# Performance work log

Hardware: AMD Instinct MI355X
Metric: run time of the kernel (lower is better)

## Reference

```python
import jax, jax.numpy as jnp
import numpy as np
from jax import lax

LR, SB, LB = 256, 16, 8  # lr_size, spatial_bin, luma_bins
DN = ('NCHW', 'OIHW', 'NCHW')


def conv2d(x, w, b=None, stride=1, pad=1):
    out = lax.conv_general_dilated(x, w, (stride, stride), [(pad, pad), (pad, pad)], dimension_numbers=DN)
    return out if b is None else out + b[None, :, None, None]


def gaussian_blur17(x):
    # kornia GaussianBlur2d(kernel=(17,17), sigma=(2,2)), reflect padding, separable
    t = jnp.arange(17, dtype=x.dtype) - 8.0
    g = jnp.exp(-(t * t) / 8.0)  # 2*sigma^2 = 8
    g = g / g.sum()
    C = x.shape[1]
    xp = jnp.pad(x, ((0, 0), (0, 0), (8, 8), (8, 8)), mode='reflect')
    kh = jnp.broadcast_to(g.reshape(1, 1, 17, 1), (C, 1, 17, 1))
    kw = jnp.broadcast_to(g.reshape(1, 1, 1, 17), (C, 1, 1, 17))
    x1 = lax.conv_general_dilated(xp, kh, (1, 1), 'VALID', dimension_numbers=DN, feature_group_count=C)
    return lax.conv_general_dilated(x1, kw, (1, 1), 'VALID', dimension_numbers=DN, feature_group_count=C)


def nearest_resize(x, size):
    # torch F.interpolate mode='nearest': src = floor(dst * in/out)
    H, W = x.shape[-2], x.shape[-1]
    iy = jnp.floor(jnp.arange(size) * (H / size)).astype(jnp.int32)
    ix = jnp.floor(jnp.arange(size) * (W / size)).astype(jnp.int32)
    return x[:, :, iy][:, :, :, ix]


def grid_sample_3d_border(inp, grid):
    # inp [B,C,D,Hi,Wi]; grid [B,Do,Ho,Wo,3] with (x,y,z); bilinear, padding_mode='border', align_corners=False
    B, C, D, Hi, Wi = inp.shape
    x = jnp.clip(((grid[..., 0] + 1.0) * Wi - 1.0) * 0.5, 0.0, Wi - 1.0)
    y = jnp.clip(((grid[..., 1] + 1.0) * Hi - 1.0) * 0.5, 0.0, Hi - 1.0)
    z = jnp.clip(((grid[..., 2] + 1.0) * D - 1.0) * 0.5, 0.0, D - 1.0)
    x0 = jnp.floor(x); y0 = jnp.floor(y); z0 = jnp.floor(z)
    fx = (x - x0)[:, None]; fy = (y - y0)[:, None]; fz = (z - z0)[:, None]  # [B,1,Do,Ho,Wo]
    x0i = x0.astype(jnp.int32); y0i = y0.astype(jnp.int32); z0i = z0.astype(jnp.int32)
    x1i = jnp.minimum(x0i + 1, Wi - 1); y1i = jnp.minimum(y0i + 1, Hi - 1); z1i = jnp.minimum(z0i + 1, D - 1)
    flat = inp.reshape(B, C, D * Hi * Wi)
    M = grid.shape[1] * grid.shape[2] * grid.shape[3]

    def gat(zi, yi, xi):
        idx = ((zi * Hi + yi) * Wi + xi).reshape(B, 1, M)
        v = jnp.take_along_axis(flat, jnp.broadcast_to(idx, (B, C, M)), axis=2)
        return v.reshape(B, C, grid.shape[1], grid.shape[2], grid.shape[3])

    return (gat(z0i, y0i, x0i) * (1 - fz) * (1 - fy) * (1 - fx)
            + gat(z0i, y0i, x1i) * (1 - fz) * (1 - fy) * fx
            + gat(z0i, y1i, x0i) * (1 - fz) * fy * (1 - fx)
            + gat(z0i, y1i, x1i) * (1 - fz) * fy * fx
            + gat(z1i, y0i, x0i) * fz * (1 - fy) * (1 - fx)
            + gat(z1i, y0i, x1i) * fz * (1 - fy) * fx
            + gat(z1i, y1i, x0i) * fz * fy * (1 - fx)
            + gat(z1i, y1i, x1i) * fz * fy * fx)


def _forward(lqs, evs, gw1, gb1, gw2, gb2, sw0, sb0, sw1, sb1, sw2, sb2, sw3, sb3,
             cw0, cb0, cw1, cb1, fw1, fb1, fw2, fb2, fw3, fb3, lw1, lb1, lw2, fuw, fub):
    B, _, H, W = lqs.shape
    # --- HighresStreamNet guide ---
    g = gaussian_blur17(lqs)
    g = jax.nn.relu(conv2d(g, gw1, gb1, 1, 0))
    guide = jax.nn.sigmoid(conv2d(g, gw2, gb2, 1, 0)) * 2.0 - 0.5  # [B,1,H,W]
    # --- slicing grid (x,y in (-0.5,1.5) per source, z = guide) ---
    gx = (jnp.arange(W, dtype=lqs.dtype) + 0.5) / W * 2.0 - 0.5
    gy = (jnp.arange(H, dtype=lqs.dtype) + 0.5) / H * 2.0 - 0.5
    gyy, gxx = jnp.meshgrid(gy, gx, indexing='ij')
    base = jnp.broadcast_to(jnp.stack([gxx, gyy], -1)[None, None], (B, 1, H, W, 2))
    grid = jnp.concatenate([base, guide[..., None]], axis=-1)  # [B,1,H,W,3]
    # --- LowresStreamNet ---
    lr = nearest_resize(lqs, LR)
    ev = evs if (evs.shape[-1] == LR and evs.shape[-2] == LR) else nearest_resize(evs, LR)
    x = jnp.concatenate([lr, ev], axis=1)  # [B,18,256,256]
    for w_, b_ in ((sw0, sb0), (sw1, sb1), (sw2, sb2), (sw3, sb3)):
        x = jax.nn.relu(conv2d(x, w_, b_, 2, 1))  # -> [B,64,16,16]
    xl = conv2d(jax.nn.relu(conv2d(x, lw1, lb1, 1, 1)), lw2, None, 1, 1)  # local, last conv no bias
    xg = jax.nn.relu(conv2d(x, cw0, cb0, 2, 1))
    xg = jax.nn.relu(conv2d(xg, cw1, cb1, 2, 1)).reshape(B, -1)  # [B,1024]
    xg = jax.nn.relu(xg @ fw1.T + fb1)
    xg = jax.nn.relu(xg @ fw2.T + fb2)
    xg = xg @ fw3.T + fb3  # [B,64]
    fused = jax.nn.relu(xg[:, :, None, None] + xl)
    bg = conv2d(fused, fuw, fub, 1, 0).reshape(B, 1, LB, SB, SB)  # bilateral grid [B,1,8,16,16]
    hr = grid_sample_3d_border(bg, grid)  # [B,1,1,H,W]
    return hr.reshape(B, -1, H, W)


def setup_inputs():
    key = jax.random.key(0)
    ks = iter(jax.random.split(key, 40))

    def W_(shape):
        fan_in = int(np.prod(shape[1:]))
        return jax.random.normal(next(ks), shape, jnp.float32) * np.float32(np.sqrt(2.0 / fan_in))

    def Z(n):
        return jnp.zeros((n,), jnp.float32)

    B, H, Wd = 8, 1024, 1024
    return {
        'lqs': jax.random.uniform(next(ks), (B, 3, H, Wd), jnp.float32),
        'evs': jax.random.normal(next(ks), (B, 15, 256, 256), jnp.float32) * 0.1,
        'gw1': W_((16, 3, 1, 1)), 'gb1': Z(16), 'gw2': W_((1, 16, 1, 1)), 'gb2': Z(1),
        'sw0': W_((8, 18, 3, 3)), 'sb0': Z(8), 'sw1': W_((16, 8, 3, 3)), 'sb1': Z(16),
        'sw2': W_((32, 16, 3, 3)), 'sb2': Z(32), 'sw3': W_((64, 32, 3, 3)), 'sb3': Z(64),
        'cw0': W_((64, 64, 3, 3)), 'cb0': Z(64), 'cw1': W_((64, 64, 3, 3)), 'cb1': Z(64),
        'fw1': W_((256, 1024)), 'fb1': Z(256), 'fw2': W_((128, 256)), 'fb2': Z(128),
        'fw3': W_((64, 128)), 'fb3': Z(64),
        'lw1': W_((64, 64, 3, 3)), 'lb1': Z(64), 'lw2': W_((64, 64, 3, 3)),
        'fuw': W_((8, 64, 1, 1)), 'fub': Z(8),
    }


def reference(lqs, evs, gw1, gb1, gw2, gb2, sw0, sb0, sw1, sb1, sw2, sb2, sw3, sb3,
              cw0, cb0, cw1, cb1, fw1, fb1, fw2, fb2, fw3, fb3, lw1, lb1, lw2, fuw, fub):
    return _forward(lqs, evs, gw1, gb1, gw2, gb2, sw0, sb0, sw1, sb1, sw2, sb2, sw3, sb3,
                    cw0, cb0, cw1, cb1, fw1, fb1, fw2, fb2, fw3, fb3, lw1, lb1, lw2, fuw, fub)
```

## Files before the change

### kernel.cpp

```cpp
#include <hip/hip_runtime.h>
#include <hip/hip_bf16.h>
#include <math.h>

#define BATCH 8
#define HH 1024
#define WW 1024

__device__ __forceinline__ int reflect1024(int i) {
    i = i < 0 ? -i : i;
    return i > 1023 ? 2046 - i : i;
}

__global__ __launch_bounds__(256) void conv0_k(const float* __restrict__ lqs,
                                               const float* __restrict__ evs,
                                               const float* __restrict__ w,
                                               const float* __restrict__ bias,
                                               float* __restrict__ out) {
    int idx = blockIdx.x * 256 + threadIdx.x;
    int q = idx & 4095;
    int b = idx >> 12;
    int qx = q & 31, oy = q >> 5;
    int iy0 = oy * 2 - 1;

    float acc[4][8];
#pragma unroll
    for (int j = 0; j < 4; ++j)
#pragma unroll
        for (int o = 0; o < 8; ++o) acc[j][o] = bias[o];

#pragma unroll
    for (int ic = 0; ic < 3; ++ic) {
        const float* ipc = lqs + (size_t)(b * 3 + ic) * HH * WW;
#pragma unroll
        for (int ky = 0; ky < 3; ++ky) {
            int iy = iy0 + ky;
            if (iy < 0) continue;
            const float* row = ipc + (size_t)iy * 4 * WW;
            float xr[9];
#pragma unroll
            for (int i = 0; i < 9; ++i) {
                int ix = 8 * qx - 1 + i;
                xr[i] = (ix >= 0) ? row[ix * 4] : 0.0f;
            }
#pragma unroll
            for (int o = 0; o < 8; ++o) {
                const float* wp = w + (o * 18 + ic) * 9 + ky * 3;
#pragma unroll
                for (int j = 0; j < 4; ++j)
#pragma unroll
                    for (int kx = 0; kx < 3; ++kx)
                        acc[j][o] = fmaf(wp[kx], xr[2 * j + kx], acc[j][o]);
            }
        }
    }
    for (int ic = 0; ic < 15; ++ic) {
        const float* ipc = evs + (size_t)(b * 15 + ic) * 65536;
#pragma unroll
        for (int ky = 0; ky < 3; ++ky) {
            int iy = iy0 + ky;
            if (iy < 0) continue;
            const float* row = ipc + iy * 256;
            const float4* r4 = (const float4*)row;
            float4 A = r4[2 * qx];
            float4 Bv = r4[2 * qx + 1];
            float m = (qx > 0) ? row[8 * qx - 1] : 0.0f;
            float xr[9] = {m, A.x, A.y, A.z, A.w, Bv.x, Bv.y, Bv.z, Bv.w};
#pragma unroll
            for (int o = 0; o < 8; ++o) {
                const float* wp = w + (o * 18 + ic + 3) * 9 + ky * 3;
#pragma unroll
                for (int j = 0; j < 4; ++j)
#pragma unroll
                    for (int kx = 0; kx < 3; ++kx)
                        acc[j][o] = fmaf(wp[kx], xr[2 * j + kx], acc[j][o]);
            }
        }
    }
#pragma unroll
    for (int o = 0; o < 8; ++o) {
        float4 v = make_float4(fmaxf(acc[0][o], 0.0f), fmaxf(acc[1][o], 0.0f),
                               fmaxf(acc[2][o], 0.0f), fmaxf(acc[3][o], 0.0f));
        *(float4*)(out + ((size_t)(b * 8 + o) << 14) + oy * 128 + qx * 4) = v;
    }
}

template <int IC, int OC, int OCT, int IH, int IW, int STRIDE, bool RELU, bool HASB>
__global__ __launch_bounds__(256) void convN_k(const float* __restrict__ in,
                                               const float* __restrict__ w,
                                               const float* __restrict__ bias,
                                               float* __restrict__ out) {
    constexpr int OH = (IH + 2 - 3) / STRIDE + 1;
    constexpr int OW = (IW + 2 - 3) / STRIDE + 1;
    constexpr int POS = OH * OW;
    constexpr int G = OC / OCT;
    int idx = blockIdx.x * 256 + threadIdx.x;
    if (idx >= BATCH * G * POS) return;
    int px = idx % POS;
    int g = (idx / POS) % G;
    int b = idx / (POS * G);
    int ox = px % OW, oy = px / OW;
    int iy0 = oy * STRIDE - 1, ix0 = ox * STRIDE - 1;

    float acc[OCT];
#pragma unroll
    for (int o = 0; o < OCT; ++o) acc[o] = HASB ? bias[g * OCT + o] : 0.0f;

    const float* ip = in + (size_t)b * IC * IH * IW;
    for (int ic = 0; ic < IC; ++ic) {
        const float* ipc = ip + ic * IH * IW;
        float x[9];
#pragma unroll
        for (int ky = 0; ky < 3; ++ky) {
            int iy = iy0 + ky;
#pragma unroll
            for (int kx = 0; kx < 3; ++kx) {
                int ix = ix0 + kx;
                bool ok = (iy >= 0) && (iy < IH) && (ix >= 0) && (ix < IW);
                x[ky * 3 + kx] = ok ? ipc[iy * IW + ix] : 0.0f;
            }
        }
#pragma unroll
        for (int o = 0; o < OCT; ++o) {
            const float* wp = w + ((g * OCT + o) * IC + ic) * 9;
#pragma unroll
            for (int k = 0; k < 9; ++k) acc[o] = fmaf(wp[k], x[k], acc[o]);
        }
    }
#pragma unroll
    for (int o = 0; o < OCT; ++o) {
        float v = acc[o];
        if (RELU) v = fmaxf(v, 0.0f);
        out[(size_t)(b * OC + g * OCT + o) * POS + px] = v;
    }
}

template <int IC, int OC, int OCT, int IH, int IW, int STRIDE, int SPLIT>
__global__ __launch_bounds__(256) void convS_k(const float* __restrict__ in,
                                               const float* __restrict__ w,
                                               float* __restrict__ part) {
    constexpr int OH = (IH + 2 - 3) / STRIDE + 1;
    constexpr int OW = (IW + 2 - 3) / STRIDE + 1;
    constexpr int POS = OH * OW;
    constexpr int G = OC / OCT;
    constexpr int TOT = BATCH * G * POS;
    constexpr int ICS = IC / SPLIT;
    constexpr int N = BATCH * OC * POS;
    int idx = blockIdx.x * 256 + threadIdx.x;
    if (idx >= TOT * SPLIT) return;
    int s = idx / TOT, r = idx % TOT;
    int px = r % POS;
    int g = (r / POS) % G;
    int b = r / (POS * G);
    int ox = px % OW, oy = px / OW;
    int iy0 = oy * STRIDE - 1, ix0 = ox * STRIDE - 1;

    float acc[OCT];
#pragma unroll
    for (int o = 0; o < OCT; ++o) acc[o] = 0.0f;

    const float* ip = in + (size_t)b * IC * IH * IW;
    for (int ic = s * ICS; ic < (s + 1) * ICS; ++ic) {
        const float* ipc = ip + ic * IH * IW;
        float x[9];
#pragma unroll
        for (int ky = 0; ky < 3; ++ky) {
            int iy = iy0 + ky;
#pragma unroll
            for (int kx = 0; kx < 3; ++kx) {
                int ix = ix0 + kx;
                bool ok = (iy >= 0) && (iy < IH) && (ix >= 0) && (ix < IW);
                x[ky * 3 + kx] = ok ? ipc[iy * IW + ix] : 0.0f;
            }
        }
#pragma unroll
        for (int o = 0; o < OCT; ++o) {
            const float* wp = w + ((g * OCT + o) * IC + ic) * 9;
#pragma unroll
            for (int k = 0; k < 9; ++k) acc[o] = fmaf(wp[k], x[k], acc[o]);
        }
    }
#pragma unroll
    for (int o = 0; o < OCT; ++o)
        part[(size_t)s * N + (size_t)(b * OC + g * OCT + o) * POS + px] = acc[o];
}

template <int OC, int POS, int SPLIT, bool RELU, bool HASB>
__global__ __launch_bounds__(256) void reduce_k(const float* __restrict__ part,
                                                const float* __restrict__ bias,
                                                float* __restrict__ out) {
    constexpr int N = BATCH * OC * POS;
    int idx = blockIdx.x * 256 + threadIdx.x;
    if (idx >= N) return;
    int oc = (idx / POS) % OC;
    float a = HASB ? bias[oc] : 0.0f;
#pragma unroll
    for (int s = 0; s < SPLIT; ++s) a += part[(size_t)s * N + idx];
    out[idx] = RELU ? fmaxf(a, 0.0f) : a;
}

__global__ __launch_bounds__(256) void fc1_k(const float* __restrict__ part_cw1,
                                             const float* __restrict__ cb1,
                                             const float* __restrict__ fw1,
                                             const float* __restrict__ fb1,
                                             float* __restrict__ h1) {
    __shared__ float xin[1024];
    int t = threadIdx.x;
    int b = blockIdx.x >> 6;
    int rgrp = blockIdx.x & 63;
    int wave = t >> 6, lane = t & 63;

    for (int i = t; i < 1024; i += 256) {
        float v = cb1[i >> 4];
#pragma unroll
        for (int s = 0; s < 16; ++s) v += part_cw1[s * 8192 + b * 1024 + i];
        xin[i] = fmaxf(v, 0.0f);
    }
    __syncthreads();

    int r = (rgrp << 2) | wave;
    const float4* w4 = (const float4*)(fw1 + r * 1024);
    const float4* x4 = (const float4*)xin;
    float acc = 0.0f;
#pragma unroll
    for (int jj = 0; jj < 4; ++jj) {
        float4 wv = w4[lane + 64 * jj];
        float4 xv = x4[lane + 64 * jj];
        acc = fmaf(wv.x, xv.x, acc);
        acc = fmaf(wv.y, xv.y, acc);
        acc = fmaf(wv.z, xv.z, acc);
        acc = fmaf(wv.w, xv.w, acc);
    }
#pragma unroll
    for (int m = 32; m; m >>= 1) acc += __shfl_xor(acc, m, 64);
    if (lane == 0) h1[b * 256 + r] = fmaxf(acc + fb1[r], 0.0f);
}

__global__ __launch_bounds__(256) void fc23fuse_k(const float* __restrict__ h1,
                                                  const float* __restrict__ fw2,
                                                  const float* __restrict__ fb2,
                                                  const float* __restrict__ fw3,
                                                  const float* __restrict__ fb3,
                                                  const float* __restrict__ part_lw2,
                                                  const float* __restrict__ fuw,
                                                  const float* __restrict__ fub,
                                                  float* __restrict__ bg) {
    __shared__ float h2[128];
    __shared__ float xg[64];
    int b = blockIdx.x, t = threadIdx.x;
    int wave = t >> 6, lane = t & 63;

    float4 xv1 = ((const float4*)(h1 + b * 256))[lane];
#pragma unroll 4
    for (int i = 0; i < 32; ++i) {
        int r = wave * 32 + i;
        float4 wv = ((const float4*)(fw2 + r * 256))[lane];
        float acc = fmaf(wv.x, xv1.x, fmaf(wv.y, xv1.y, fmaf(wv.z, xv1.z, wv.w * xv1.w)));
#pragma unroll
        for (int m = 32; m; m >>= 1) acc += __shfl_xor(acc, m, 64);
        if (lane == 0) h2[r] = fmaxf(acc + fb2[r], 0.0f);
    }
    __syncthreads();

    float2 xv2 = ((const float2*)h2)[lane];
#pragma unroll 4
    for (int i = 0; i < 16; ++i) {
        int r = wave * 16 + i;
        float2 wv = ((const float2*)(fw3 + r * 128))[lane];
        float acc = fmaf(wv.x, xv2.x, wv.y * xv2.y);
#pragma unroll
        for (int m = 32; m; m >>= 1) acc += __shfl_xor(acc, m, 64);
        if (lane == 0) xg[r] = acc + fb3[r];
    }
    __syncthreads();

    int px = t;
    float acc[8];
#pragma unroll
    for (int d = 0; d < 8; ++d) acc[d] = fub[d];
    for (int c = 0; c < 64; ++c) {
        int base = (b * 64 + c) * 256 + px;
        float xlv = 0.0f;
#pragma unroll
        for (int s = 0; s < 8; ++s) xlv += part_lw2[s * 131072 + base];
        float f = fmaxf(xg[c] + xlv, 0.0f);
#pragma unroll
        for (int d = 0; d < 8; ++d) acc[d] = fmaf(fuw[d * 64 + c], f, acc[d]);
    }
#pragma unroll
    for (int d = 0; d < 8; ++d) bg[(b * 8 + d) * 256 + px] = acc[d];
}

__global__ __launch_bounds__(256) void guide_slice_k(const float* __restrict__ lqs,
                                                     const float* __restrict__ bgp,
                                                     const float* __restrict__ gw1,
                                                     const float* __restrict__ gb1,
                                                     const float* __restrict__ gw2,
                                                     const float* __restrict__ gb2,
                                                     float* __restrict__ out) {
    constexpr int TW = 64, TH = 32;
    __shared__ float sBH[3][TH][81];
    __shared__ float sBG[2048];
    __shared__ float sW1[48], sB1[16], sW2[16], sB2v[1];

    int t = threadIdx.x;
    int bx = blockIdx.x & 15;
    int by = (blockIdx.x >> 4) & 31;
    int b = blockIdx.x >> 9;
    int x0 = bx * TW, y0 = by * TH;

    float gv[17];
    {
        float gs = 0.0f;
#pragma unroll
        for (int i = 0; i < 17; ++i) {
            float d = (float)i - 8.0f;
            gv[i] = expf(-(d * d) * 0.125f);
            gs += gv[i];
        }
        float inv = 1.0f / gs;
#pragma unroll
        for (int i = 0; i < 17; ++i) gv[i] *= inv;
    }

    for (int i = t; i < 2048; i += 256) sBG[i] = bgp[b * 2048 + i];
    if (t < 48) sW1[t] = gw1[t];
    if (t < 16) { sB1[t] = gb1[t]; sW2[t] = gw2[t]; }
    if (t == 0) sB2v[0] = gb2[0];

    if (t < 240) {
        int c = t / 80, xo = t % 80;
        int gx = reflect1024(x0 + xo - 8);
        const float* colp = lqs + (size_t)(b * 3 + c) * HH * WW + gx;
        float win[17];
#pragma unroll
        for (int i = 0; i < 16; ++i)
            win[i] = colp[(size_t)reflect1024(y0 - 8 + i) * WW];
#pragma unroll
        for (int j = 0; j < TH; ++j) {
            win[(16 + j) % 17] = colp[(size_t)reflect1024(y0 + 8 + j) * WW];
            float acc = 0.0f;
#pragma unroll
            for (int i = 0; i < 17; ++i) acc = fmaf(gv[i], win[(j + i) % 17], acc);
            sBH[c][j][xo] = acc;
        }
    }
    __syncthreads();

    int yy = t >> 3, xs = (t & 7) * 8;
    int Y = y0 + yy;
    float fy = fminf(fmaxf((Y + 0.5f) * (1.0f / 64.0f) + 3.5f, 0.0f), 15.0f);
    float yf = floorf(fy);
    int yi = (int)yf;
    float ay = fy - yf;
    int yi1 = min(yi + 1, 15);

    float bcv[3][8];
#pragma unroll
    for (int c = 0; c < 3; ++c) {
        float win[17];
#pragma unroll
        for (int i = 0; i < 16; ++i) win[i] = sBH[c][yy][xs + i];
#pragma unroll
        for (int j = 0; j < 8; ++j) {
            win[(16 + j) % 17] = sBH[c][yy][xs + 16 + j];
            float acc = 0.0f;
#pragma unroll
            for (int i = 0; i < 17; ++i) acc = fmaf(gv[i], win[(j + i) % 17], acc);
            bcv[c][j] = acc;
        }
    }

    float val[8];
#pragma unroll
    for (int j = 0; j < 8; ++j) {
        float b0 = bcv[0][j], b1 = bcv[1][j], b2 = bcv[2][j];
        float s = sB2v[0];
#pragma unroll
        for (int c = 0; c < 16; ++c) {
            float g1 = fmaf(sW1[c * 3 + 0], b0,
                       fmaf(sW1[c * 3 + 1], b1,
                       fmaf(sW1[c * 3 + 2], b2, sB1[c])));
            s = fmaf(sW2[c], fmaxf(g1, 0.0f), s);
        }
        float sig = 1.0f / (1.0f + expf(-s));
        float guide = sig * 2.0f - 0.5f;

        int X = x0 + xs + j;
        float fx = fminf(fmaxf((X + 0.5f) * (1.0f / 64.0f) + 3.5f, 0.0f), 15.0f);
        float fz = fminf(fmaxf(fmaf(guide, 4.0f, 3.5f), 0.0f), 7.0f);
        float xf = floorf(fx), zf = floorf(fz);
        int xi = (int)xf, zi = (int)zf;
        float ax = fx - xf, az = fz - zf;
        int xi1 = min(xi + 1, 15), zi1 = min(zi + 1, 7);

        const float* g0 = sBG + zi * 256;
        const float* g1p = sBG + zi1 * 256;
        int i00 = yi * 16 + xi, i01 = yi * 16 + xi1;
        int i10 = yi1 * 16 + xi, i11 = yi1 * 16 + xi1;
        float c00 = g0[i00] + az * (g1p[i00] - g0[i00]);
        float c01 = g0[i01] + az * (g1p[i01] - g0[i01]);
        float c10 = g0[i10] + az * (g1p[i10] - g0[i10]);
        float c11 = g0[i11] + az * (g1p[i11] - g0[i11]);
        float c0 = c00 + ay * (c10 - c00);
        float c1 = c01 + ay * (c11 - c01);
        val[j] = c0 + ax * (c1 - c0);
    }
    float4* op = (float4*)(out + (size_t)b * HH * WW + (size_t)Y * WW + x0 + xs);
    op[0] = make_float4(val[0], val[1], val[2], val[3]);
    op[1] = make_float4(val[4], val[5], val[6], val[7]);
}

extern "C" void kernel_launch(void* const* d_in, const int* in_sizes, int n_in,
                              void* d_out, int out_size, void* d_ws, size_t ws_size,
                              hipStream_t stream) {
    const float* lqs = (const float*)d_in[0];
    const float* evs = (const float*)d_in[1];
    const float* gw1 = (const float*)d_in[2];
    const float* gb1 = (const float*)d_in[3];
    const float* gw2 = (const float*)d_in[4];
    const float* gb2 = (const float*)d_in[5];
    const float* sw0 = (const float*)d_in[6];
    const float* sb0 = (const float*)d_in[7];
    const float* sw1 = (const float*)d_in[8];
    const float* sb1 = (const float*)d_in[9];
    const float* sw2 = (const float*)d_in[10];
    const float* sb2 = (const float*)d_in[11];
    const float* sw3 = (const float*)d_in[12];
    const float* sb3 = (const float*)d_in[13];
    const float* cw0 = (const float*)d_in[14];
    const float* cb0 = (const float*)d_in[15];
    const float* cw1 = (const float*)d_in[16];
    const float* cb1 = (const float*)d_in[17];
    const float* fw1 = (const float*)d_in[18];
    const float* fb1 = (const float*)d_in[19];
    const float* fw2 = (const float*)d_in[20];
    const float* fb2 = (const float*)d_in[21];
    const float* fw3 = (const float*)d_in[22];
    const float* fb3 = (const float*)d_in[23];
    const float* lw1 = (const float*)d_in[24];
    const float* lb1 = (const float*)d_in[25];
    const float* lw2 = (const float*)d_in[26];
    const float* fuw = (const float*)d_in[27];
    const float* fub = (const float*)d_in[28];
    float* out = (float*)d_out;

    float* ws = (float*)d_ws;
    float* o0 = ws;
    float* o1 = o0 + 1048576;
    float* o2 = o1 + 524288;
    float* o3 = o2 + 262144;
    float* xl1 = o3 + 131072;
    float* xg0 = xl1 + 131072;
    float* h1 = xg0 + 32768;
    float* bg = h1 + 2048;
    float* partA = bg + 16384;
    float* part_lw2 = partA + 1048576;
    float* part_cw1 = part_lw2 + 1048576;

    conv0_k<<<128, 256, 0, stream>>>(lqs, evs, sw0, sb0, o0);
    convN_k<8, 16, 8, 128, 128, 2, true, true><<<256, 256, 0, stream>>>(o0, sw1, sb1, o1);
    convS_k<16, 32, 8, 64, 64, 2, 4><<<512, 256, 0, stream>>>(o1, sw2, partA);
    reduce_k<32, 1024, 4, true, true><<<1024, 256, 0, stream>>>(partA, sb2, o2);
    convS_k<32, 64, 8, 32, 32, 2, 8><<<512, 256, 0, stream>>>(o2, sw3, partA);
    reduce_k<64, 256, 8, true, true><<<512, 256, 0, stream>>>(partA, sb3, o3);
    convS_k<64, 64, 8, 16, 16, 1, 8><<<512, 256, 0, stream>>>(o3, lw1, partA);
    reduce_k<64, 256, 8, true, true><<<512, 256, 0, stream>>>(partA, lb1, xl1);
    convS_k<64, 64, 8, 16, 16, 1, 8><<<512, 256, 0, stream>>>(xl1, lw2, part_lw2);
    convS_k<64, 64, 8, 16, 16, 2, 16><<<256, 256, 0, stream>>>(o3, cw0, partA);
    reduce_k<64, 64, 16, true, true><<<128, 256, 0, stream>>>(partA, cb0, xg0);
    convS_k<64, 64, 4, 8, 8, 2, 16><<<128, 256, 0, stream>>>(xg0, cw1, part_cw1);
    fc1_k<<<512, 256, 0, stream>>>(part_cw1, cb1, fw1, fb1, h1);
    fc23fuse_k<<<8, 256, 0, stream>>>(h1, fw2, fb2, fw3, fb3, part_lw2, fuw, fub, bg);
    guide_slice_k<<<BATCH * 32 * 16, 256, 0, stream>>>(lqs, bg, gw1, gb1, gw2, gb2, out);
}
```

Before: 431.2 us.

## Fuse pipeline into persistent megakernel with grid barriers and overlapped guide blur

Replaces the fifteen separate launches with one persistent kernel of 768 blocks that walks the stages, separated by a software grid barrier built on atomics. The expensive 17x17 blur and guide MLP move out of the final slice kernel and are spread across the early, under-filled conv stages, so they overlap with the small convolutions. The guide z-coordinate is stored as a 16-bit fixed-point value and read back by a lighter slice pass. This removes launch gaps and idle tails. In exchange it adds barrier cost, depends on all 768 blocks being co-resident to avoid deadlock, loses some precision from the z quantization, and adds the extra global write and read of the quantized guide.

```diff
diff --git a/kernel.cpp b/kernel.cpp
--- a/kernel.cpp
+++ b/kernel.cpp
@@ -5,18 +5,37 @@
 #define BATCH 8
 #define HH 1024
 #define WW 1024
+#define NB 768
 
 __device__ __forceinline__ int reflect1024(int i) {
     i = i < 0 ? -i : i;
     return i > 1023 ? 2046 - i : i;
 }
 
-__global__ __launch_bounds__(256) void conv0_k(const float* __restrict__ lqs,
-                                               const float* __restrict__ evs,
-                                               const float* __restrict__ w,
-                                               const float* __restrict__ bias,
-                                               float* __restrict__ out) {
-    int idx = blockIdx.x * 256 + threadIdx.x;
+__device__ __forceinline__ void gridbar(unsigned int* cnt, unsigned int* gen) {
+    __syncthreads();
+    if (threadIdx.x == 0) {
+        __threadfence();
+        unsigned int g = atomicAdd(gen, 0u);
+        unsigned int a = atomicAdd(cnt, 1u);
+        if (a == NB - 1) {
+            atomicExch(cnt, 0u);
+            __threadfence();
+            atomicAdd(gen, 1u);
+        } else {
+            while (atomicAdd(gen, 0u) == g) __builtin_amdgcn_s_sleep(16);
+        }
+        __threadfence();
+    }
+    __syncthreads();
+}
+
+__device__ __forceinline__ void dev_conv0(int idx,
+                                          const float* __restrict__ lqs,
+                                          const float* __restrict__ evs,
+                                          const float* __restrict__ w,
+                                          const float* __restrict__ bias,
+                                          float* __restrict__ out) {
     int q = idx & 4095;
     int b = idx >> 12;
     int qx = q & 31, oy = q >> 5;
@@ -85,15 +104,15 @@
 }
 
 template <int IC, int OC, int OCT, int IH, int IW, int STRIDE, bool RELU, bool HASB>
-__global__ __launch_bounds__(256) void convN_k(const float* __restrict__ in,
-                                               const float* __restrict__ w,
-                                               const float* __restrict__ bias,
-                                               float* __restrict__ out) {
+__device__ __forceinline__ void dev_convN(int idx,
+                                          const float* __restrict__ in,
+                                          const float* __restrict__ w,
+                                          const float* __restrict__ bias,
+                                          float* __restrict__ out) {
     constexpr int OH = (IH + 2 - 3) / STRIDE + 1;
     constexpr int OW = (IW + 2 - 3) / STRIDE + 1;
     constexpr int POS = OH * OW;
     constexpr int G = OC / OCT;
-    int idx = blockIdx.x * 256 + threadIdx.x;
     if (idx >= BATCH * G * POS) return;
     int px = idx % POS;
     int g = (idx / POS) % G;
@@ -135,9 +154,10 @@
 }
 
 template <int IC, int OC, int OCT, int IH, int IW, int STRIDE, int SPLIT>
-__global__ __launch_bounds__(256) void convS_k(const float* __restrict__ in,
-                                               const float* __restrict__ w,
-                                               float* __restrict__ part) {
+__device__ __forceinline__ void dev_convS(int idx,
+                                          const float* __restrict__ in,
+                                          const float* __restrict__ w,
+                                          float* __restrict__ part) {
     constexpr int OH = (IH + 2 - 3) / STRIDE + 1;
     constexpr int OW = (IW + 2 - 3) / STRIDE + 1;
     constexpr int POS = OH * OW;
@@ -145,7 +165,6 @@
     constexpr int TOT = BATCH * G * POS;
     constexpr int ICS = IC / SPLIT;
     constexpr int N = BATCH * OC * POS;
-    int idx = blockIdx.x * 256 + threadIdx.x;
     if (idx >= TOT * SPLIT) return;
     int s = idx / TOT, r = idx % TOT;
     int px = r % POS;
@@ -185,11 +204,11 @@
 }
 
 template <int OC, int POS, int SPLIT, bool RELU, bool HASB>
-__global__ __launch_bounds__(256) void reduce_k(const float* __restrict__ part,
-                                                const float* __restrict__ bias,
-                                                float* __restrict__ out) {
+__device__ __forceinline__ void dev_reduce(int idx,
+                                           const float* __restrict__ part,
+                                           const float* __restrict__ bias,
+                                           float* __restrict__ out) {
     constexpr int N = BATCH * OC * POS;
-    int idx = blockIdx.x * 256 + threadIdx.x;
     if (idx >= N) return;
     int oc = (idx / POS) % OC;
     float a = HASB ? bias[oc] : 0.0f;
@@ -198,21 +217,118 @@
     out[idx] = RELU ? fmaxf(a, 0.0f) : a;
 }
 
-__global__ __launch_bounds__(256) void fc1_k(const float* __restrict__ part_cw1,
-                                             const float* __restrict__ cb1,
-                                             const float* __restrict__ fw1,
-                                             const float* __restrict__ fb1,
-                                             float* __restrict__ h1) {
-    __shared__ float xin[1024];
-    int t = threadIdx.x;
-    int b = blockIdx.x >> 6;
-    int rgrp = blockIdx.x & 63;
+__device__ __forceinline__ void dev_blur(int tile, int t,
+                                         const float* __restrict__ lqs,
+                                         const float* __restrict__ gw1,
+                                         const float* __restrict__ gb1,
+                                         const float* __restrict__ gw2,
+                                         const float* __restrict__ gb2,
+                                         unsigned short* __restrict__ gq,
+                                         float* sm) {
+    float* sBH = sm;
+    float* sW1 = sm + 7776;
+    float* sB1 = sW1 + 48;
+    float* sW2 = sB1 + 16;
+    float* sB2v = sW2 + 16;
+    __syncthreads();
+
+    int bx = tile & 15;
+    int by = (tile >> 4) & 31;
+    int b = tile >> 9;
+    int x0 = bx * 64, y0 = by * 32;
+
+    float gv[17];
+    {
+        float gs = 0.0f;
+#pragma unroll
+        for (int i = 0; i < 17; ++i) {
+            float d = (float)i - 8.0f;
+            gv[i] = expf(-(d * d) * 0.125f);
+            gs += gv[i];
+        }
+        float inv = 1.0f / gs;
+#pragma unroll
+        for (int i = 0; i < 17; ++i) gv[i] *= inv;
+    }
+
+    if (t < 48) sW1[t] = gw1[t];
+    if (t < 16) { sB1[t] = gb1[t]; sW2[t] = gw2[t]; }
+    if (t == 0) sB2v[0] = gb2[0];
+
+    if (t < 240) {
+        int c = t / 80, xo = t % 80;
+        int gx = reflect1024(x0 + xo - 8);
+        const float* colp = lqs + (size_t)(b * 3 + c) * HH * WW + gx;
+        float win[17];
+#pragma unroll
+        for (int i = 0; i < 16; ++i)
+            win[i] = colp[(size_t)reflect1024(y0 - 8 + i) * WW];
+#pragma unroll
+        for (int j = 0; j < 32; ++j) {
+            win[(16 + j) % 17] = colp[(size_t)reflect1024(y0 + 8 + j) * WW];
+            float acc = 0.0f;
+#pragma unroll
+            for (int i = 0; i < 17; ++i) acc = fmaf(gv[i], win[(j + i) % 17], acc);
+            sBH[(c * 32 + j) * 81 + xo] = acc;
+        }
+    }
+    __syncthreads();
+
+    int yy = t >> 3, xs = (t & 7) * 8;
+    float bcv[3][8];
+#pragma unroll
+    for (int c = 0; c < 3; ++c) {
+        float win[17];
+#pragma unroll
+        for (int i = 0; i < 16; ++i) win[i] = sBH[(c * 32 + yy) * 81 + xs + i];
+#pragma unroll
+        for (int j = 0; j < 8; ++j) {
+            win[(16 + j) % 17] = sBH[(c * 32 + yy) * 81 + xs + 16 + j];
+            float acc = 0.0f;
+#pragma unroll
+            for (int i = 0; i < 17; ++i) acc = fmaf(gv[i], win[(j + i) % 17], acc);
+            bcv[c][j] = acc;
+        }
+    }
+
+    unsigned int qw[4];
+#pragma unroll
+    for (int j = 0; j < 8; ++j) {
+        float b0 = bcv[0][j], b1 = bcv[1][j], b2 = bcv[2][j];
+        float s = sB2v[0];
+#pragma unroll
+        for (int c = 0; c < 16; ++c) {
+            float g1 = fmaf(sW1[c * 3 + 0], b0,
+                       fmaf(sW1[c * 3 + 1], b1,
+                       fmaf(sW1[c * 3 + 2], b2, sB1[c])));
+            s = fmaf(sW2[c], fmaxf(g1, 0.0f), s);
+        }
+        float sig = 1.0f / (1.0f + expf(-s));
+        float guide = sig * 2.0f - 0.5f;
+        float fz = fminf(fmaxf(fmaf(guide, 4.0f, 3.5f), 0.0f), 7.0f);
+        unsigned int q = (unsigned int)(fz * 8192.0f + 0.5f);
+        if (j & 1) qw[j >> 1] |= (q << 16);
+        else qw[j >> 1] = q;
+    }
+    size_t o = ((size_t)b << 20) + ((size_t)(y0 + yy) << 10) + x0 + xs;
+    *(uint4*)(gq + o) = make_uint4(qw[0], qw[1], qw[2], qw[3]);
+}
+
+__device__ __forceinline__ void dev_fc1(int w, int t,
+                                        const float* __restrict__ partD,
+                                        const float* __restrict__ cb1,
+                                        const float* __restrict__ fw1,
+                                        const float* __restrict__ fb1,
+                                        float* __restrict__ h1, float* sm) {
+    float* xin = sm;
+    __syncthreads();
+    int b = w >> 6, rgrp = w & 63;
     int wave = t >> 6, lane = t & 63;
 
     for (int i = t; i < 1024; i += 256) {
         float v = cb1[i >> 4];
 #pragma unroll
-        for (int s = 0; s < 16; ++s) v += part_cw1[s * 8192 + b * 1024 + i];
+        for (int s = 0; s < 16; ++s) v += partD[s * 8192 + b * 1024 + i];
         xin[i] = fmaxf(v, 0.0f);
     }
     __syncthreads();
@@ -235,18 +351,20 @@
     if (lane == 0) h1[b * 256 + r] = fmaxf(acc + fb1[r], 0.0f);
 }
 
-__global__ __launch_bounds__(256) void fc23fuse_k(const float* __restrict__ h1,
-                                                  const float* __restrict__ fw2,
-                                                  const float* __restrict__ fb2,
-                                                  const float* __restrict__ fw3,
-                                                  const float* __restrict__ fb3,
-                                                  const float* __restrict__ part_lw2,
-                                                  const float* __restrict__ fuw,
-                                                  const float* __restrict__ fub,
-                                                  float* __restrict__ bg) {
-    __shared__ float h2[128];
-    __shared__ float xg[64];
-    int b = blockIdx.x, t = threadIdx.x;
+__device__ __forceinline__ void dev_fc23fuse(int w, int t,
+                                             const float* __restrict__ h1,
+                                             const float* __restrict__ fw2,
+                                             const float* __restrict__ fb2,
+                                             const float* __restrict__ fw3,
+                                             const float* __restrict__ fb3,
+                                             const float* __restrict__ partC,
+                                             const float* __restrict__ fuw,
+                                             const float* __restrict__ fub,
+                                             float* __restrict__ bg, float* sm) {
+    float* h2 = sm;
+    float* xg = sm + 128;
+    __syncthreads();
+    int b = w >> 3, d = w & 7;
     int wave = t >> 6, lane = t & 63;
 
     float4 xv1 = ((const float4*)(h1 + b * 256))[lane];
@@ -274,120 +392,46 @@
     __syncthreads();
 
     int px = t;
-    float acc[8];
-#pragma unroll
-    for (int d = 0; d < 8; ++d) acc[d] = fub[d];
+    float acc = fub[d];
     for (int c = 0; c < 64; ++c) {
         int base = (b * 64 + c) * 256 + px;
         float xlv = 0.0f;
 #pragma unroll
-        for (int s = 0; s < 8; ++s) xlv += part_lw2[s * 131072 + base];
+        for (int s = 0; s < 8; ++s) xlv += partC[s * 131072 + base];
         float f = fmaxf(xg[c] + xlv, 0.0f);
-#pragma unroll
-        for (int d = 0; d < 8; ++d) acc[d] = fmaf(fuw[d * 64 + c], f, acc[d]);
-    }
-#pragma unroll
-    for (int d = 0; d < 8; ++d) bg[(b * 8 + d) * 256 + px] = acc[d];
-}
-
-__global__ __launch_bounds__(256) void guide_slice_k(const float* __restrict__ lqs,
-                                                     const float* __restrict__ bgp,
-                                                     const float* __restrict__ gw1,
-                                                     const float* __restrict__ gb1,
-                                                     const float* __restrict__ gw2,
-                                                     const float* __restrict__ gb2,
-                                                     float* __restrict__ out) {
-    constexpr int TW = 64, TH = 32;
-    __shared__ float sBH[3][TH][81];
-    __shared__ float sBG[2048];
-    __shared__ float sW1[48], sB1[16], sW2[16], sB2v[1];
-
-    int t = threadIdx.x;
-    int bx = blockIdx.x & 15;
-    int by = (blockIdx.x >> 4) & 31;
-    int b = blockIdx.x >> 9;
-    int x0 = bx * TW, y0 = by * TH;
-
-    float gv[17];
-    {
-        float gs = 0.0f;
-#pragma unroll
-        for (int i = 0; i < 17; ++i) {
-            float d = (float)i - 8.0f;
-            gv[i] = expf(-(d * d) * 0.125f);
-            gs += gv[i];
-        }
-        float inv = 1.0f / gs;
-#pragma unroll
-        for (int i = 0; i < 17; ++i) gv[i] *= inv;
-    }
-
+        acc = fmaf(fuw[d * 64 + c], f, acc);
+    }
+    bg[(b * 8 + d) * 256 + px] = acc;
+}
+
+__device__ __forceinline__ void dev_slice(int w, int t,
+                                          const unsigned short* __restrict__ gq,
+                                          const float* __restrict__ bgp,
+                                          float* __restrict__ out, float* sm) {
+    float* sBG = sm;
+    __syncthreads();
+    int b = w >> 9;
     for (int i = t; i < 2048; i += 256) sBG[i] = bgp[b * 2048 + i];
-    if (t < 48) sW1[t] = gw1[t];
-    if (t < 16) { sB1[t] = gb1[t]; sW2[t] = gw2[t]; }
-    if (t == 0) sB2v[0] = gb2[0];
-
-    if (t < 240) {
-        int c = t / 80, xo = t % 80;
-        int gx = reflect1024(x0 + xo - 8);
-        const float* colp = lqs + (size_t)(b * 3 + c) * HH * WW + gx;
-        float win[17];
-#pragma unroll
-        for (int i = 0; i < 16; ++i)
-            win[i] = colp[(size_t)reflect1024(y0 - 8 + i) * WW];
-#pragma unroll
-        for (int j = 0; j < TH; ++j) {
-            win[(16 + j) % 17] = colp[(size_t)reflect1024(y0 + 8 + j) * WW];
-            float acc = 0.0f;
-#pragma unroll
-            for (int i = 0; i < 17; ++i) acc = fmaf(gv[i], win[(j + i) % 17], acc);
-            sBH[c][j][xo] = acc;
-        }
-    }
-    __syncthreads();
-
-    int yy = t >> 3, xs = (t & 7) * 8;
-    int Y = y0 + yy;
+    __syncthreads();
+
+    int off = (w & 511) * 2048 + t * 8;
+    int Y = off >> 10, X0 = off & 1023;
     float fy = fminf(fmaxf((Y + 0.5f) * (1.0f / 64.0f) + 3.5f, 0.0f), 15.0f);
     float yf = floorf(fy);
     int yi = (int)yf;
     float ay = fy - yf;
     int yi1 = min(yi + 1, 15);
 
-    float bcv[3][8];
-#pragma unroll
-    for (int c = 0; c < 3; ++c) {
-        float win[17];
-#pragma unroll
-        for (int i = 0; i < 16; ++i) win[i] = sBH[c][yy][xs + i];
-#pragma unroll
-        for (int j = 0; j < 8; ++j) {
-            win[(16 + j) % 17] = sBH[c][yy][xs + 16 + j];
-            float acc = 0.0f;
-#pragma unroll
-            for (int i = 0; i < 17; ++i) acc = fmaf(gv[i], win[(j + i) % 17], acc);
-            bcv[c][j] = acc;
-        }
-    }
+    uint4 qv = *(const uint4*)(gq + ((size_t)b << 20) + off);
+    unsigned int qw[4] = {qv.x, qv.y, qv.z, qv.w};
 
     float val[8];
 #pragma unroll
     for (int j = 0; j < 8; ++j) {
-        float b0 = bcv[0][j], b1 = bcv[1][j], b2 = bcv[2][j];
-        float s = sB2v[0];
-#pragma unroll
-        for (int c = 0; c < 16; ++c) {
-            float g1 = fmaf(sW1[c * 3 + 0], b0,
-                       fmaf(sW1[c * 3 + 1], b1,
-                       fmaf(sW1[c * 3 + 2], b2, sB1[c])));
-            s = fmaf(sW2[c], fmaxf(g1, 0.0f), s);
-        }
-        float sig = 1.0f / (1.0f + expf(-s));
-        float guide = sig * 2.0f - 0.5f;
-
-        int X = x0 + xs + j;
+        unsigned int q = (qw[j >> 1] >> ((j & 1) * 16)) & 0xffff;
+        float fz = (float)q * (1.0f / 8192.0f);
+        int X = X0 + j;
         float fx = fminf(fmaxf((X + 0.5f) * (1.0f / 64.0f) + 3.5f, 0.0f), 15.0f);
-        float fz = fminf(fmaxf(fmaf(guide, 4.0f, 3.5f), 0.0f), 7.0f);
         float xf = floorf(fx), zf = floorf(fz);
         int xi = (int)xf, zi = (int)zf;
         float ax = fx - xf, az = fz - zf;
@@ -405,9 +449,90 @@
         float c1 = c01 + ay * (c11 - c01);
         val[j] = c0 + ax * (c1 - c0);
     }
-    float4* op = (float4*)(out + (size_t)b * HH * WW + (size_t)Y * WW + x0 + xs);
+    float4* op = (float4*)(out + ((size_t)b << 20) + off);
     op[0] = make_float4(val[0], val[1], val[2], val[3]);
     op[1] = make_float4(val[4], val[5], val[6], val[7]);
+}
+
+__global__ __launch_bounds__(256, 4) void mega_k(
+    const float* __restrict__ lqs, const float* __restrict__ evs,
+    const float* __restrict__ gw1, const float* __restrict__ gb1,
+    const float* __restrict__ gw2, const float* __restrict__ gb2,
+    const float* __restrict__ sw0, const float* __restrict__ sb0,
+    const float* __restrict__ sw1, const float* __restrict__ sb1,
+    const float* __restrict__ sw2, const float* __restrict__ sb2,
+    const float* __restrict__ sw3, const float* __restrict__ sb3,
+    const float* __restrict__ cw0, const float* __restrict__ cb0,
+    const float* __restrict__ cw1, const float* __restrict__ cb1,
+    const float* __restrict__ fw1, const float* __restrict__ fb1,
+    const float* __restrict__ fw2, const float* __restrict__ fb2,
+    const float* __restrict__ fw3, const float* __restrict__ fb3,
+    const float* __restrict__ lw1, const float* __restrict__ lb1,
+    const float* __restrict__ lw2,
+    const float* __restrict__ fuw, const float* __restrict__ fub,
+    float* __restrict__ o0, float* __restrict__ o1, float* __restrict__ o2,
+    float* __restrict__ o3, float* __restrict__ xl1, float* __restrict__ xg0,
+    float* __restrict__ h1, float* __restrict__ bg,
+    float* __restrict__ partA, float* __restrict__ partB,
+    float* __restrict__ partC, float* __restrict__ partD,
+    unsigned short* __restrict__ gq, float* __restrict__ out,
+    unsigned int* bar) {
+    extern __shared__ float sm[];
+    int blk = blockIdx.x, t = threadIdx.x;
+    unsigned int* cnt = bar;
+    unsigned int* gen = bar + 1;
+
+    for (int w = blk; w < 1408; w += NB) {
+        if (w < 128) dev_conv0(w * 256 + t, lqs, evs, sw0, sb0, o0);
+        else dev_blur(w - 128, t, lqs, gw1, gb1, gw2, gb2, gq, sm);
+    }
+    gridbar(cnt, gen);
+    for (int w = blk; w < 1536; w += NB) {
+        if (w < 256) dev_convN<8, 16, 8, 128, 128, 2, true, true>(w * 256 + t, o0, sw1, sb1, o1);
+        else dev_blur(1280 + w - 256, t, lqs, gw1, gb1, gw2, gb2, gq, sm);
+    }
+    gridbar(cnt, gen);
+    for (int w = blk; w < 1024; w += NB) {
+        if (w < 512) dev_convS<16, 32, 8, 64, 64, 2, 4>(w * 256 + t, o1, sw2, partA);
+        else dev_blur(2560 + w - 512, t, lqs, gw1, gb1, gw2, gb2, gq, sm);
+    }
+    gridbar(cnt, gen);
+    for (int w = blk; w < 1024; w += NB)
+        dev_reduce<32, 1024, 4, true, true>(w * 256 + t, partA, sb2, o2);
+    gridbar(cnt, gen);
+    for (int w = blk; w < 1024; w += NB) {
+        if (w < 512) dev_convS<32, 64, 8, 32, 32, 2, 8>(w * 256 + t, o2, sw3, partA);
+        else dev_blur(3072 + w - 512, t, lqs, gw1, gb1, gw2, gb2, gq, sm);
+    }
+    gridbar(cnt, gen);
+    for (int w = blk; w < 1024; w += NB) {
+        if (w < 512) dev_reduce<64, 256, 8, true, true>(w * 256 + t, partA, sb3, o3);
+        else dev_blur(3584 + w - 512, t, lqs, gw1, gb1, gw2, gb2, gq, sm);
+    }
+    gridbar(cnt, gen);
+    for (int w = blk; w < 768; w += NB) {
+        if (w < 512) dev_convS<64, 64, 8, 16, 16, 1, 8>(w * 256 + t, o3, lw1, partA);
+        else dev_convS<64, 64, 8, 16, 16, 2, 16>((w - 512) * 256 + t, o3, cw0, partB);
+    }
+    gridbar(cnt, gen);
+    for (int w = blk; w < 640; w += NB) {
+        if (w < 512) dev_reduce<64, 256, 8, true, true>(w * 256 + t, partA, lb1, xl1);
+        else dev_reduce<64, 64, 16, true, true>((w - 512) * 256 + t, partB, cb0, xg0);
+    }
+    gridbar(cnt, gen);
+    for (int w = blk; w < 640; w += NB) {
+        if (w < 512) dev_convS<64, 64, 8, 16, 16, 1, 8>(w * 256 + t, xl1, lw2, partC);
+        else dev_convS<64, 64, 4, 8, 8, 2, 16>((w - 512) * 256 + t, xg0, cw1, partD);
+    }
+    gridbar(cnt, gen);
+    for (int w = blk; w < 512; w += NB)
+        dev_fc1(w, t, partD, cb1, fw1, fb1, h1, sm);
+    gridbar(cnt, gen);
+    for (int w = blk; w < 64; w += NB)
+        dev_fc23fuse(w, t, h1, fw2, fb2, fw3, fb3, partC, fuw, fub, bg, sm);
+    gridbar(cnt, gen);
+    for (int w = blk; w < 4096; w += NB)
+        dev_slice(w, t, gq, bg, out, sm);
 }
 
 extern "C" void kernel_launch(void* const* d_in, const int* in_sizes, int n_in,
@@ -454,22 +579,16 @@
     float* h1 = xg0 + 32768;
     float* bg = h1 + 2048;
     float* partA = bg + 16384;
-    float* part_lw2 = partA + 1048576;
-    float* part_cw1 = part_lw2 + 1048576;
-
-    conv0_k<<<128, 256, 0, stream>>>(lqs, evs, sw0, sb0, o0);
-    convN_k<8, 16, 8, 128, 128, 2, true, true><<<256, 256, 0, stream>>>(o0, sw1, sb1, o1);
-    convS_k<16, 32, 8, 64, 64, 2, 4><<<512, 256, 0, stream>>>(o1, sw2, partA);
-    reduce_k<32, 1024, 4, true, true><<<1024, 256, 0, stream>>>(partA, sb2, o2);
-    convS_k<32, 64, 8, 32, 32, 2, 8><<<512, 256, 0, stream>>>(o2, sw3, partA);
-    reduce_k<64, 256, 8, true, true><<<512, 256, 0, stream>>>(partA, sb3, o3);
-    convS_k<64, 64, 8, 16, 16, 1, 8><<<512, 256, 0, stream>>>(o3, lw1, partA);
-    reduce_k<64, 256, 8, true, true><<<512, 256, 0, stream>>>(partA, lb1, xl1);
-    convS_k<64, 64, 8, 16, 16, 1, 8><<<512, 256, 0, stream>>>(xl1, lw2, part_lw2);
-    convS_k<64, 64, 8, 16, 16, 2, 16><<<256, 256, 0, stream>>>(o3, cw0, partA);
-    reduce_k<64, 64, 16, true, true><<<128, 256, 0, stream>>>(partA, cb0, xg0);
-    convS_k<64, 64, 4, 8, 8, 2, 16><<<128, 256, 0, stream>>>(xg0, cw1, part_cw1);
-    fc1_k<<<512, 256, 0, stream>>>(part_cw1, cb1, fw1, fb1, h1);
-    fc23fuse_k<<<8, 256, 0, stream>>>(h1, fw2, fb2, fw3, fb3, part_lw2, fuw, fub, bg);
-    guide_slice_k<<<BATCH * 32 * 16, 256, 0, stream>>>(lqs, bg, gw1, gb1, gw2, gb2, out);
-}
+    float* partB = partA + 1048576;
+    float* partC = partB + 524288;
+    float* partD = partC + 1048576;
+    unsigned int* bar = (unsigned int*)(partD + 131072);
+    unsigned short* gq = (unsigned short*)(bar + 4);
+
+    hipMemsetAsync(bar, 0, 16, stream);
+    mega_k<<<NB, 256, 31488, stream>>>(
+        lqs, evs, gw1, gb1, gw2, gb2, sw0, sb0, sw1, sb1, sw2, sb2, sw3, sb3,
+        cw0, cb0, cw1, cb1, fw1, fb1, fw2, fb2, fw3, fb3, lw1, lb1, lw2,
+        fuw, fub, o0, o1, o2, o3, xl1, xg0, h1, bg,
+        partA, partB, partC, partD, gq, out, bar);
+}
```

New measurement: 1.649 ms. 3.82x slower.
